# Optimization experiments

Hardware: AMD Instinct MI355X
Metric: run time of the kernel (lower is better)

Reference implementation:

```python
import math
import jax, jax.numpy as jnp
import numpy as np

B, L, S, H, E = 4, 2048, 2048, 8, 64

def setup_inputs() -> dict:
    key = jax.random.key(0)
    kq, kk, kv, km = jax.random.split(key, 4)
    queries = jax.random.normal(kq, (B, L, H, E), dtype=jnp.float32)
    keys = jax.random.normal(kk, (B, S, H, E), dtype=jnp.float32)
    values = jax.random.normal(kv, (B, S, H, E), dtype=jnp.float32)
    # bool mask [B, L, S]; True => masked out (filled with -10000)
    attn_mask = jax.random.randint(km, (B, L, S), 0, 2).astype(bool)
    return {"queries": queries, "keys": keys, "values": values, "attn_mask": attn_mask}

def reference(queries, keys, values, attn_mask):
    # queries: [B,L,H,E], keys/values: [B,S,H,E], attn_mask: [B,L,S] bool
    Edim = queries.shape[-1]
    scale = 1.0 / math.sqrt(Edim)  # self.scale is None -> 1/sqrt(E)
    scores = jnp.einsum('blhe,bshe->bhls', queries, keys) * scale  # [B,H,L,S]
    scores = jnp.where(attn_mask[:, None, :, :], jnp.float32(-10000.0), scores)
    A = jax.nn.softmax(scores, axis=-1)  # dropout is identity at eval time
    V = jnp.einsum('bhls,bshd->blhd', A, values)  # [B,L,H,E]
    return V, A
```

## Files before the change

kernel.cpp:

```cpp
#include <hip/hip_runtime.h>


typedef __attribute__((ext_vector_type(8))) short bf16x8;
typedef __attribute__((ext_vector_type(4))) short bf16x4;
typedef __attribute__((ext_vector_type(4))) float f32x4;

#define NB 4
#define NL 2048
#define NS 2048
#define NH 8
#define NE 64
#define SKC 64
#define SC2 0.18033688011112042f
#define MB2 -5.770780163555854f
#define EXP2(x) __builtin_amdgcn_exp2f(x)

static __device__ __forceinline__ short f2bf(float x) {
  unsigned u = __builtin_bit_cast(unsigned, x);
  u += 0x7fffu + ((u >> 16) & 1u);
  return (short)(u >> 16);
}

static __device__ __forceinline__ bf16x8 pack8(f32x4 a, f32x4 b) {
  bf16x8 t;
  t[0] = f2bf(a[0]); t[1] = f2bf(a[1]); t[2] = f2bf(a[2]); t[3] = f2bf(a[3]);
  t[4] = f2bf(b[0]); t[5] = f2bf(b[1]); t[6] = f2bf(b[2]); t[7] = f2bf(b[3]);
  return t;
}

__global__ __launch_bounds__(256)
void prep_all(const float* __restrict__ K, const float* __restrict__ V,
              const int* __restrict__ M, short* __restrict__ Kb,
              short* __restrict__ Vt, unsigned long long* __restrict__ Mb) {
  __shared__ short t_lds[64 * 65];
  const int bid = blockIdx.x, tid = threadIdx.x;
  if (bid < 4096) {
    long i4 = ((long)bid * 256 + tid) * 4;
    f32x4 v = *(const f32x4*)(K + i4);
    int e4 = (int)(i4 & 63);
    long r = i4 >> 6;
    int h = (int)(r & 7);
    long r2 = r >> 3;
    int t = (int)(r2 & 2047);
    int b = (int)(r2 >> 11);
    bf16x4 o;
    o[0] = f2bf(v[0]); o[1] = f2bf(v[1]); o[2] = f2bf(v[2]); o[3] = f2bf(v[3]);
    *(bf16x4*)(Kb + ((((long)b * NH + h) * NL + t) * NE + e4)) = o;
  } else if (bid < 5120) {
    const int vb = bid - 4096;
    const int b = vb >> 8;
    const int h = (vb >> 5) & 7;
    const int sb = (vb & 31) * 64;
    {
      const int s = tid >> 2, e0 = (tid & 3) * 16;
      const float* vp = V + ((((long)b * NS + sb + s) * NH + h) * NE + e0);
      #pragma unroll
      for (int j = 0; j < 4; ++j) {
        f32x4 u = *(const f32x4*)(vp + j * 4);
        #pragma unroll
        for (int r = 0; r < 4; ++r) t_lds[(e0 + j * 4 + r) * 65 + s] = f2bf(u[r]);
      }
    }
    __syncthreads();
    {
      const int e = tid >> 2, s0 = (tid & 3) * 16;
      short* op = Vt + (((long)b * NH + h) * NE + e) * NS + sb + s0;
      short tmp[16];
      #pragma unroll
      for (int j = 0; j < 16; ++j) tmp[j] = t_lds[e * 65 + s0 + j];
      *(bf16x8*)(op)     = *(bf16x8*)(tmp);
      *(bf16x8*)(op + 8) = *(bf16x8*)(tmp + 8);
    }
  } else {
    const long total = (long)NB * NL * NS;
    long g = (long)(bid - 5120) * 256 + tid;
    const long stride = 2048L * 256;
    for (; g < total; g += stride) {
      unsigned long long bal = __ballot(M[g] != 0);
      if ((tid & 63) == 0) Mb[g >> 6] = bal;
    }
  }
}


template<int RS>
static __device__ __forceinline__ void stage_tile(const short* __restrict__ base,
                                                  short* lds, int tid, int w) {
  #pragma unroll
  for (int c = 0; c < 2; ++c) {
    const int rr = (tid >> 3) + c * 32;
    const int gg = (tid & 7) ^ (rr & 7);
    const short* sp = base + (long)rr * RS + gg * 8;
    __builtin_amdgcn_global_load_lds(
        (const __attribute__((address_space(1))) void*)sp,
        (__attribute__((address_space(3))) void*)(void*)((char*)lds + c * 4096 + w * 1024),
        16, 0, 0);
  }
}

__global__ __launch_bounds__(256, 2)
void attn_main(const float* __restrict__ Qg, const short* __restrict__ Kb,
               const short* __restrict__ Vt, const unsigned long long* __restrict__ Mb,
               float* __restrict__ OutV, float* __restrict__ OutA)
{
  __shared__ short k_lds[2][SKC * 64];
  __shared__ short vt_lds[2][NE * 64];
  __shared__ short p_lds[4][16 * 64];

  const int bid = blockIdx.x;
  const int hh = bid & 7, qt = (bid >> 3) & 15, bb = bid >> 7;
  const int tid = threadIdx.x, w = tid >> 6, lane = tid & 63;
  const int lq = lane & 15, lg = lane >> 4;
  const int qwA = qt * 128 + w * 16, qrowA = qwA + lq;
  const int qwB = qwA + 64,          qrowB = qrowA + 64;

  const short* Kpan = Kb + (long)(bb * NH + hh) * NS * NE;
  const short* Vpan = Vt + (long)(bb * NH + hh) * NE * NS;

  bf16x8 qfA0, qfA1, qfB0, qfB1;
  {
    const float* qp = Qg + (((long)bb * NL + qrowA) * NH + hh) * NE + 8 * lg;
    qfA0 = pack8(*(const f32x4*)(qp),      *(const f32x4*)(qp + 4));
    qfA1 = pack8(*(const f32x4*)(qp + 32), *(const f32x4*)(qp + 36));
    const float* qpB = qp + (long)64 * NH * NE;
    qfB0 = pack8(*(const f32x4*)(qpB),      *(const f32x4*)(qpB + 4));
    qfB1 = pack8(*(const f32x4*)(qpB + 32), *(const f32x4*)(qpB + 36));
  }

  const unsigned long long* mrowA = Mb + ((long)bb * NL + qrowA) * (NS / 64);
  const unsigned long long* mrowB = Mb + ((long)bb * NL + qrowB) * (NS / 64);

  float l0 = 0.f, l1 = 0.f, l2 = 0.f, l3 = 0.f;
  stage_tile<NE>(Kpan, &k_lds[0][0], tid, w);
  __syncthreads();
  unsigned long long mcA = mrowA[0];
  for (int sb = 0; sb < NS; sb += SKC) {
    const int cb = (sb >> 6) & 1;
    if (sb + SKC < NS)
      stage_tile<NE>(Kpan + (long)(sb + SKC) * NE, &k_lds[cb ^ 1][0], tid, w);
    const unsigned long long mnA = (sb + SKC < NS) ? mrowA[(sb >> 6) + 1] : 0ULL;
    #pragma unroll
    for (int st = 0; st < SKC; st += 16) {
      const int krow = st + lq, sw = (krow & 7) << 3;
      const bf16x8 kf0 = *(const bf16x8*)&k_lds[cb][(krow * 64 + 8 * lg) ^ sw];
      const bf16x8 kf1 = *(const bf16x8*)&k_lds[cb][(krow * 64 + 32 + 8 * lg) ^ sw];
      f32x4 c = {0.f, 0.f, 0.f, 0.f};
      c = __builtin_amdgcn_mfma_f32_16x16x32_bf16(kf0, qfA0, c, 0, 0, 0);
      c = __builtin_amdgcn_mfma_f32_16x16x32_bf16(kf1, qfA1, c, 0, 0, 0);
      const unsigned mb4 = (unsigned)(mcA >> (st + 4 * lg)) & 0xFu;
      l0 += (mb4 & 1u) ? 0.f : EXP2(fmaf(c[0], SC2, MB2));
      l1 += (mb4 & 2u) ? 0.f : EXP2(fmaf(c[1], SC2, MB2));
      l2 += (mb4 & 4u) ? 0.f : EXP2(fmaf(c[2], SC2, MB2));
      l3 += (mb4 & 8u) ? 0.f : EXP2(fmaf(c[3], SC2, MB2));
    }
    mcA = mnA;
    __syncthreads();
  }
  float lA = (l0 + l1) + (l2 + l3);
  lA += __shfl_xor(lA, 16, 64);
  lA += __shfl_xor(lA, 32, 64);
  const float rinvA = 1.0f / lA;

  f32x4 accvA[4];
  #pragma unroll
  for (int et = 0; et < 4; ++et) accvA[et] = (f32x4){0.f, 0.f, 0.f, 0.f};
  l0 = l1 = l2 = l3 = 0.f;

  float* arowA = OutA + (((long)(bb * NH + hh)) * NL + qrowA) * NS;

  stage_tile<NE>(Kpan, &k_lds[0][0], tid, w);
  stage_tile<NS>(Vpan, &vt_lds[0][0], tid, w);
  __syncthreads();
  mcA = mrowA[0];
  unsigned long long mcB = mrowB[0];
  for (int sb = 0; sb < NS; sb += SKC) {
    const int cb = (sb >> 6) & 1;
    if (sb + SKC < NS) {
      stage_tile<NE>(Kpan + (long)(sb + SKC) * NE, &k_lds[cb ^ 1][0], tid, w);
      stage_tile<NS>(Vpan + (sb + SKC), &vt_lds[cb ^ 1][0], tid, w);
    }
    const unsigned long long mnA = (sb + SKC < NS) ? mrowA[(sb >> 6) + 1] : 0ULL;
    const unsigned long long mnB = (sb + SKC < NS) ? mrowB[(sb >> 6) + 1] : 0ULL;
    #pragma unroll
    for (int st = 0; st < SKC; st += 16) {
      const int krow = st + lq, sw = (krow & 7) << 3;
      const bf16x8 kf0 = *(const bf16x8*)&k_lds[cb][(krow * 64 + 8 * lg) ^ sw];
      const bf16x8 kf1 = *(const bf16x8*)&k_lds[cb][(krow * 64 + 32 + 8 * lg) ^ sw];
      f32x4 cA = {0.f, 0.f, 0.f, 0.f};
      cA = __builtin_amdgcn_mfma_f32_16x16x32_bf16(kf0, qfA0, cA, 0, 0, 0);
      cA = __builtin_amdgcn_mfma_f32_16x16x32_bf16(kf1, qfA1, cA, 0, 0, 0);
      f32x4 cB = {0.f, 0.f, 0.f, 0.f};
      cB = __builtin_amdgcn_mfma_f32_16x16x32_bf16(kf0, qfB0, cB, 0, 0, 0);
      cB = __builtin_amdgcn_mfma_f32_16x16x32_bf16(kf1, qfB1, cB, 0, 0, 0);
      const unsigned mA4 = (unsigned)(mcA >> (st + 4 * lg)) & 0xFu;
      const float p0 = (mA4 & 1u) ? 0.f : EXP2(fmaf(cA[0], SC2, MB2));
      const float p1 = (mA4 & 2u) ? 0.f : EXP2(fmaf(cA[1], SC2, MB2));
      const float p2 = (mA4 & 4u) ? 0.f : EXP2(fmaf(cA[2], SC2, MB2));
      const float p3 = (mA4 & 8u) ? 0.f : EXP2(fmaf(cA[3], SC2, MB2));
      const float a0 = p0 * rinvA, a1 = p1 * rinvA, a2 = p2 * rinvA, a3 = p3 * rinvA;
      f32x4 av = {a0, a1, a2, a3};
      __builtin_nontemporal_store(av, (f32x4*)(arowA + sb + st + 4 * lg));
      bf16x4 pv;
      pv[0] = f2bf(a0); pv[1] = f2bf(a1); pv[2] = f2bf(a2); pv[3] = f2bf(a3);
      *(bf16x4*)&p_lds[w][(lq * 64 + st + 4 * lg) ^ ((lq & 7) << 3)] = pv;
      const unsigned mB4 = (unsigned)(mcB >> (st + 4 * lg)) & 0xFu;
      l0 += (mB4 & 1u) ? 0.f : EXP2(fmaf(cB[0], SC2, MB2));
      l1 += (mB4 & 2u) ? 0.f : EXP2(fmaf(cB[1], SC2, MB2));
      l2 += (mB4 & 4u) ? 0.f : EXP2(fmaf(cB[2], SC2, MB2));
      l3 += (mB4 & 8u) ? 0.f : EXP2(fmaf(cB[3], SC2, MB2));
    }
    #pragma unroll
    for (int kc2 = 0; kc2 < 2; ++kc2) {
      const bf16x8 pf = *(const bf16x8*)&p_lds[w][(lq * 64 + kc2 * 32 + 8 * lg) ^ ((lq & 7) << 3)];
      #pragma unroll
      for (int et = 0; et < 4; ++et) {
        const int er = et * 16 + lq;
        const bf16x8 vf = *(const bf16x8*)&vt_lds[cb][(er * 64 + kc2 * 32 + 8 * lg) ^ ((er & 7) << 3)];
        accvA[et] = __builtin_amdgcn_mfma_f32_16x16x32_bf16(pf, vf, accvA[et], 0, 0, 0);
      }
    }
    mcA = mnA; mcB = mnB;
    __syncthreads();
  }
  float lB = (l0 + l1) + (l2 + l3);
  lB += __shfl_xor(lB, 16, 64);
  lB += __shfl_xor(lB, 32, 64);
  const float rinvB = 1.0f / lB;

  {
    float* vout = OutV + (((long)bb * NL + qwA + 4 * lg) * NH + hh) * NE + lq;
    #pragma unroll
    for (int r = 0; r < 4; ++r)
      #pragma unroll
      for (int et = 0; et < 4; ++et)
        vout[(long)r * (NH * NE) + et * 16] = accvA[et][r];
  }

  f32x4 accvB[4];
  #pragma unroll
  for (int et = 0; et < 4; ++et) accvB[et] = (f32x4){0.f, 0.f, 0.f, 0.f};

  float* arowB = OutA + (((long)(bb * NH + hh)) * NL + qrowB) * NS;

  stage_tile<NE>(Kpan, &k_lds[0][0], tid, w);
  stage_tile<NS>(Vpan, &vt_lds[0][0], tid, w);
  __syncthreads();
  mcB = mrowB[0];
  for (int sb = 0; sb < NS; sb += SKC) {
    const int cb = (sb >> 6) & 1;
    if (sb + SKC < NS) {
      stage_tile<NE>(Kpan + (long)(sb + SKC) * NE, &k_lds[cb ^ 1][0], tid, w);
      stage_tile<NS>(Vpan + (sb + SKC), &vt_lds[cb ^ 1][0], tid, w);
    }
    const unsigned long long mnB = (sb + SKC < NS) ? mrowB[(sb >> 6) + 1] : 0ULL;
    #pragma unroll
    for (int st = 0; st < SKC; st += 16) {
      const int krow = st + lq, sw = (krow & 7) << 3;
      const bf16x8 kf0 = *(const bf16x8*)&k_lds[cb][(krow * 64 + 8 * lg) ^ sw];
      const bf16x8 kf1 = *(const bf16x8*)&k_lds[cb][(krow * 64 + 32 + 8 * lg) ^ sw];
      f32x4 c = {0.f, 0.f, 0.f, 0.f};
      c = __builtin_amdgcn_mfma_f32_16x16x32_bf16(kf0, qfB0, c, 0, 0, 0);
      c = __builtin_amdgcn_mfma_f32_16x16x32_bf16(kf1, qfB1, c, 0, 0, 0);
      const unsigned mb4 = (unsigned)(mcB >> (st + 4 * lg)) & 0xFu;
      const float p0 = (mb4 & 1u) ? 0.f : EXP2(fmaf(c[0], SC2, MB2));
      const float p1 = (mb4 & 2u) ? 0.f : EXP2(fmaf(c[1], SC2, MB2));
      const float p2 = (mb4 & 4u) ? 0.f : EXP2(fmaf(c[2], SC2, MB2));
      const float p3 = (mb4 & 8u) ? 0.f : EXP2(fmaf(c[3], SC2, MB2));
      const float a0 = p0 * rinvB, a1 = p1 * rinvB, a2 = p2 * rinvB, a3 = p3 * rinvB;
      f32x4 av = {a0, a1, a2, a3};
      __builtin_nontemporal_store(av, (f32x4*)(arowB + sb + st + 4 * lg));
      bf16x4 pv;
      pv[0] = f2bf(a0); pv[1] = f2bf(a1); pv[2] = f2bf(a2); pv[3] = f2bf(a3);
      *(bf16x4*)&p_lds[w][(lq * 64 + st + 4 * lg) ^ ((lq & 7) << 3)] = pv;
    }
    #pragma unroll
    for (int kc2 = 0; kc2 < 2; ++kc2) {
      const bf16x8 pf = *(const bf16x8*)&p_lds[w][(lq * 64 + kc2 * 32 + 8 * lg) ^ ((lq & 7) << 3)];
      #pragma unroll
      for (int et = 0; et < 4; ++et) {
        const int er = et * 16 + lq;
        const bf16x8 vf = *(const bf16x8*)&vt_lds[cb][(er * 64 + kc2 * 32 + 8 * lg) ^ ((er & 7) << 3)];
        accvB[et] = __builtin_amdgcn_mfma_f32_16x16x32_bf16(pf, vf, accvB[et], 0, 0, 0);
      }
    }
    mcB = mnB;
    __syncthreads();
  }

  {
    float* vout = OutV + (((long)bb * NL + qwB + 4 * lg) * NH + hh) * NE + lq;
    #pragma unroll
    for (int r = 0; r < 4; ++r)
      #pragma unroll
      for (int et = 0; et < 4; ++et)
        vout[(long)r * (NH * NE) + et * 16] = accvB[et][r];
  }
}

extern "C" void kernel_launch(void* const* d_in, const int* in_sizes, int n_in,
                              void* d_out, int out_size, void* d_ws, size_t ws_size,
                              hipStream_t stream) {
  const float* Q = (const float*)d_in[0];
  const float* K = (const float*)d_in[1];
  const float* V = (const float*)d_in[2];
  const int*   M = (const int*)d_in[3];
  float* outv = (float*)d_out;
  float* outa = outv + (size_t)NB * NL * NH * NE;

  const size_t NQK = (size_t)NB * NH * NL * NE;
  short* Kbw = (short*)d_ws;
  short* Vtw = Kbw + NQK;
  unsigned long long* Mbp = (unsigned long long*)(Vtw + NQK);

  prep_all<<<dim3(7168), 256, 0, stream>>>(K, V, M, Kbw, Vtw, Mbp);
  attn_main<<<dim3(NB * (NL / 128) * NH), 256, 0, stream>>>(Q, Kbw, Vtw, Mbp, outv, outa);
}
```

Before: 203.1 us.

## Load K and V fragments directly from global memory instead of LDS staging

Removes the double-buffered LDS staging of K and V tiles (global_load_lds plus block barriers) and has each lane read its bf16 MFMA fragments straight from global memory through the cache. This drops the per-iteration __syncthreads and LDS traffic, so warps no longer wait on each other. In exchange every wave re-fetches the same K/V data from L1/L2 with no explicit prefetch, which may expose load latency and raise cache pressure.

```diff
diff --git a/kernel.cpp b/kernel.cpp
--- a/kernel.cpp
+++ b/kernel.cpp
@@ -83,28 +83,11 @@
 }
 
 
-template<int RS>
-static __device__ __forceinline__ void stage_tile(const short* __restrict__ base,
-                                                  short* lds, int tid, int w) {
-  #pragma unroll
-  for (int c = 0; c < 2; ++c) {
-    const int rr = (tid >> 3) + c * 32;
-    const int gg = (tid & 7) ^ (rr & 7);
-    const short* sp = base + (long)rr * RS + gg * 8;
-    __builtin_amdgcn_global_load_lds(
-        (const __attribute__((address_space(1))) void*)sp,
-        (__attribute__((address_space(3))) void*)(void*)((char*)lds + c * 4096 + w * 1024),
-        16, 0, 0);
-  }
-}
-
 __global__ __launch_bounds__(256, 2)
 void attn_main(const float* __restrict__ Qg, const short* __restrict__ Kb,
                const short* __restrict__ Vt, const unsigned long long* __restrict__ Mb,
                float* __restrict__ OutV, float* __restrict__ OutA)
 {
-  __shared__ short k_lds[2][SKC * 64];
-  __shared__ short vt_lds[2][NE * 64];
   __shared__ short p_lds[4][16 * 64];
 
   const int bid = blockIdx.x;
@@ -116,6 +99,9 @@
 
   const short* Kpan = Kb + (long)(bb * NH + hh) * NS * NE;
   const short* Vpan = Vt + (long)(bb * NH + hh) * NE * NS;
+
+  const short* kfrag = Kpan + (long)lq * NE + 8 * lg;
+  const short* vfrag = Vpan + (long)lq * NS + 8 * lg;
 
   bf16x8 qfA0, qfA1, qfB0, qfB1;
   {
@@ -131,19 +117,13 @@
   const unsigned long long* mrowB = Mb + ((long)bb * NL + qrowB) * (NS / 64);
 
   float l0 = 0.f, l1 = 0.f, l2 = 0.f, l3 = 0.f;
-  stage_tile<NE>(Kpan, &k_lds[0][0], tid, w);
-  __syncthreads();
-  unsigned long long mcA = mrowA[0];
   for (int sb = 0; sb < NS; sb += SKC) {
-    const int cb = (sb >> 6) & 1;
-    if (sb + SKC < NS)
-      stage_tile<NE>(Kpan + (long)(sb + SKC) * NE, &k_lds[cb ^ 1][0], tid, w);
-    const unsigned long long mnA = (sb + SKC < NS) ? mrowA[(sb >> 6) + 1] : 0ULL;
+    const unsigned long long mcA = mrowA[sb >> 6];
     #pragma unroll
     for (int st = 0; st < SKC; st += 16) {
-      const int krow = st + lq, sw = (krow & 7) << 3;
-      const bf16x8 kf0 = *(const bf16x8*)&k_lds[cb][(krow * 64 + 8 * lg) ^ sw];
-      const bf16x8 kf1 = *(const bf16x8*)&k_lds[cb][(krow * 64 + 32 + 8 * lg) ^ sw];
+      const short* kp = kfrag + (long)(sb + st) * NE;
+      const bf16x8 kf0 = *(const bf16x8*)(kp);
+      const bf16x8 kf1 = *(const bf16x8*)(kp + 32);
       f32x4 c = {0.f, 0.f, 0.f, 0.f};
       c = __builtin_amdgcn_mfma_f32_16x16x32_bf16(kf0, qfA0, c, 0, 0, 0);
       c = __builtin_amdgcn_mfma_f32_16x16x32_bf16(kf1, qfA1, c, 0, 0, 0);
@@ -153,8 +133,6 @@
       l2 += (mb4 & 4u) ? 0.f : EXP2(fmaf(c[2], SC2, MB2));
       l3 += (mb4 & 8u) ? 0.f : EXP2(fmaf(c[3], SC2, MB2));
     }
-    mcA = mnA;
-    __syncthreads();
   }
   float lA = (l0 + l1) + (l2 + l3);
   lA += __shfl_xor(lA, 16, 64);
@@ -168,24 +146,14 @@
 
   float* arowA = OutA + (((long)(bb * NH + hh)) * NL + qrowA) * NS;
 
-  stage_tile<NE>(Kpan, &k_lds[0][0], tid, w);
-  stage_tile<NS>(Vpan, &vt_lds[0][0], tid, w);
-  __syncthreads();
-  mcA = mrowA[0];
-  unsigned long long mcB = mrowB[0];
   for (int sb = 0; sb < NS; sb += SKC) {
-    const int cb = (sb >> 6) & 1;
-    if (sb + SKC < NS) {
-      stage_tile<NE>(Kpan + (long)(sb + SKC) * NE, &k_lds[cb ^ 1][0], tid, w);
-      stage_tile<NS>(Vpan + (sb + SKC), &vt_lds[cb ^ 1][0], tid, w);
-    }
-    const unsigned long long mnA = (sb + SKC < NS) ? mrowA[(sb >> 6) + 1] : 0ULL;
-    const unsigned long long mnB = (sb + SKC < NS) ? mrowB[(sb >> 6) + 1] : 0ULL;
+    const unsigned long long mcA = mrowA[sb >> 6];
+    const unsigned long long mcB = mrowB[sb >> 6];
     #pragma unroll
     for (int st = 0; st < SKC; st += 16) {
-      const int krow = st + lq, sw = (krow & 7) << 3;
-      const bf16x8 kf0 = *(const bf16x8*)&k_lds[cb][(krow * 64 + 8 * lg) ^ sw];
-      const bf16x8 kf1 = *(const bf16x8*)&k_lds[cb][(krow * 64 + 32 + 8 * lg) ^ sw];
+      const short* kp = kfrag + (long)(sb + st) * NE;
+      const bf16x8 kf0 = *(const bf16x8*)(kp);
+      const bf16x8 kf1 = *(const bf16x8*)(kp + 32);
       f32x4 cA = {0.f, 0.f, 0.f, 0.f};
       cA = __builtin_amdgcn_mfma_f32_16x16x32_bf16(kf0, qfA0, cA, 0, 0, 0);
       cA = __builtin_amdgcn_mfma_f32_16x16x32_bf16(kf1, qfA1, cA, 0, 0, 0);
@@ -214,13 +182,10 @@
       const bf16x8 pf = *(const bf16x8*)&p_lds[w][(lq * 64 + kc2 * 32 + 8 * lg) ^ ((lq & 7) << 3)];
       #pragma unroll
       for (int et = 0; et < 4; ++et) {
-        const int er = et * 16 + lq;
-        const bf16x8 vf = *(const bf16x8*)&vt_lds[cb][(er * 64 + kc2 * 32 + 8 * lg) ^ ((er & 7) << 3)];
+        const bf16x8 vf = *(const bf16x8*)(vfrag + (long)(et * 16) * NS + sb + kc2 * 32);
         accvA[et] = __builtin_amdgcn_mfma_f32_16x16x32_bf16(pf, vf, accvA[et], 0, 0, 0);
       }
     }
-    mcA = mnA; mcB = mnB;
-    __syncthreads();
   }
   float lB = (l0 + l1) + (l2 + l3);
   lB += __shfl_xor(lB, 16, 64);
@@ -242,22 +207,13 @@
 
   float* arowB = OutA + (((long)(bb * NH + hh)) * NL + qrowB) * NS;
 
-  stage_tile<NE>(Kpan, &k_lds[0][0], tid, w);
-  stage_tile<NS>(Vpan, &vt_lds[0][0], tid, w);
-  __syncthreads();
-  mcB = mrowB[0];
   for (int sb = 0; sb < NS; sb += SKC) {
-    const int cb = (sb >> 6) & 1;
-    if (sb + SKC < NS) {
-      stage_tile<NE>(Kpan + (long)(sb + SKC) * NE, &k_lds[cb ^ 1][0], tid, w);
-      stage_tile<NS>(Vpan + (sb + SKC), &vt_lds[cb ^ 1][0], tid, w);
-    }
-    const unsigned long long mnB = (sb + SKC < NS) ? mrowB[(sb >> 6) + 1] : 0ULL;
+    const unsigned long long mcB = mrowB[sb >> 6];
     #pragma unroll
     for (int st = 0; st < SKC; st += 16) {
-      const int krow = st + lq, sw = (krow & 7) << 3;
-      const bf16x8 kf0 = *(const bf16x8*)&k_lds[cb][(krow * 64 + 8 * lg) ^ sw];
-      const bf16x8 kf1 = *(const bf16x8*)&k_lds[cb][(krow * 64 + 32 + 8 * lg) ^ sw];
+      const short* kp = kfrag + (long)(sb + st) * NE;
+      const bf16x8 kf0 = *(const bf16x8*)(kp);
+      const bf16x8 kf1 = *(const bf16x8*)(kp + 32);
       f32x4 c = {0.f, 0.f, 0.f, 0.f};
       c = __builtin_amdgcn_mfma_f32_16x16x32_bf16(kf0, qfB0, c, 0, 0, 0);
       c = __builtin_amdgcn_mfma_f32_16x16x32_bf16(kf1, qfB1, c, 0, 0, 0);
@@ -278,13 +234,10 @@
       const bf16x8 pf = *(const bf16x8*)&p_lds[w][(lq * 64 + kc2 * 32 + 8 * lg) ^ ((lq & 7) << 3)];
       #pragma unroll
       for (int et = 0; et < 4; ++et) {
-        const int er = et * 16 + lq;
-        const bf16x8 vf = *(const bf16x8*)&vt_lds[cb][(er * 64 + kc2 * 32 + 8 * lg) ^ ((er & 7) << 3)];
+        const bf16x8 vf = *(const bf16x8*)(vfrag + (long)(et * 16) * NS + sb + kc2 * 32);
         accvB[et] = __builtin_amdgcn_mfma_f32_16x16x32_bf16(pf, vf, accvB[et], 0, 0, 0);
       }
     }
-    mcB = mnB;
-    __syncthreads();
   }
 
   {
```

Measured after the change: 379.6 us, median of 2. 87.0% more time.

## Triple-buffer K/V LDS tiles with explicit vmcnt waits and raw barriers

Applied to the files above, without the earlier changes.

Turns the double-buffered K and V^T LDS staging into a three-stage ring with prefetch distance two in all three passes. Each iteration issues its loads after the compute and then waits with s_waitcnt vmcnt(N) plus s_barrier, so the newest tile can stay in flight, instead of a full __syncthreads drain. This aims to hide global-load latency behind MFMA and exp work. In exchange, LDS use rises by one K and one V tile per block, and the hand-counted vmcnt values must match the compiler's count of outstanding loads, including the interleaved mask and nontemporal stores, which makes the code fragile.

```diff
diff --git a/kernel.cpp b/kernel.cpp
--- a/kernel.cpp
+++ b/kernel.cpp
@@ -11,6 +11,7 @@
 #define NH 8
 #define NE 64
 #define SKC 64
+#define NT (NS / SKC)
 #define SC2 0.18033688011112042f
 #define MB2 -5.770780163555854f
 #define EXP2(x) __builtin_amdgcn_exp2f(x)
@@ -103,8 +104,8 @@
                const short* __restrict__ Vt, const unsigned long long* __restrict__ Mb,
                float* __restrict__ OutV, float* __restrict__ OutA)
 {
-  __shared__ short k_lds[2][SKC * 64];
-  __shared__ short vt_lds[2][NE * 64];
+  __shared__ short k_lds[3][SKC * 64];
+  __shared__ short vt_lds[3][NE * 64];
   __shared__ short p_lds[4][16 * 64];
 
   const int bid = blockIdx.x;
@@ -131,30 +132,39 @@
   const unsigned long long* mrowB = Mb + ((long)bb * NL + qrowB) * (NS / 64);
 
   float l0 = 0.f, l1 = 0.f, l2 = 0.f, l3 = 0.f;
-  stage_tile<NE>(Kpan, &k_lds[0][0], tid, w);
-  __syncthreads();
-  unsigned long long mcA = mrowA[0];
-  for (int sb = 0; sb < NS; sb += SKC) {
-    const int cb = (sb >> 6) & 1;
-    if (sb + SKC < NS)
-      stage_tile<NE>(Kpan + (long)(sb + SKC) * NE, &k_lds[cb ^ 1][0], tid, w);
-    const unsigned long long mnA = (sb + SKC < NS) ? mrowA[(sb >> 6) + 1] : 0ULL;
-    #pragma unroll
-    for (int st = 0; st < SKC; st += 16) {
-      const int krow = st + lq, sw = (krow & 7) << 3;
-      const bf16x8 kf0 = *(const bf16x8*)&k_lds[cb][(krow * 64 + 8 * lg) ^ sw];
-      const bf16x8 kf1 = *(const bf16x8*)&k_lds[cb][(krow * 64 + 32 + 8 * lg) ^ sw];
-      f32x4 c = {0.f, 0.f, 0.f, 0.f};
-      c = __builtin_amdgcn_mfma_f32_16x16x32_bf16(kf0, qfA0, c, 0, 0, 0);
-      c = __builtin_amdgcn_mfma_f32_16x16x32_bf16(kf1, qfA1, c, 0, 0, 0);
-      const unsigned mb4 = (unsigned)(mcA >> (st + 4 * lg)) & 0xFu;
-      l0 += (mb4 & 1u) ? 0.f : EXP2(fmaf(c[0], SC2, MB2));
-      l1 += (mb4 & 2u) ? 0.f : EXP2(fmaf(c[1], SC2, MB2));
-      l2 += (mb4 & 4u) ? 0.f : EXP2(fmaf(c[2], SC2, MB2));
-      l3 += (mb4 & 8u) ? 0.f : EXP2(fmaf(c[3], SC2, MB2));
-    }
-    mcA = mnA;
-    __syncthreads();
+  {
+    short *k0 = &k_lds[0][0], *k1 = &k_lds[1][0], *k2 = &k_lds[2][0];
+    stage_tile<NE>(Kpan, k0, tid, w);
+    stage_tile<NE>(Kpan + (long)SKC * NE, k1, tid, w);
+    asm volatile("s_waitcnt vmcnt(2)" ::: "memory");
+    __builtin_amdgcn_s_barrier();
+    unsigned long long mcA = mrowA[0];
+    for (int t = 0; t < NT; ++t) {
+      const unsigned long long mnA = mrowA[t + 1 < NT ? t + 1 : NT - 1];
+      #pragma unroll
+      for (int st = 0; st < SKC; st += 16) {
+        const int krow = st + lq, sw = (krow & 7) << 3;
+        const bf16x8 kf0 = *(const bf16x8*)&k0[(krow * 64 + 8 * lg) ^ sw];
+        const bf16x8 kf1 = *(const bf16x8*)&k0[(krow * 64 + 32 + 8 * lg) ^ sw];
+        f32x4 c = {0.f, 0.f, 0.f, 0.f};
+        c = __builtin_amdgcn_mfma_f32_16x16x32_bf16(kf0, qfA0, c, 0, 0, 0);
+        c = __builtin_amdgcn_mfma_f32_16x16x32_bf16(kf1, qfA1, c, 0, 0, 0);
+        const unsigned mb4 = (unsigned)(mcA >> (st + 4 * lg)) & 0xFu;
+        l0 += (mb4 & 1u) ? 0.f : EXP2(fmaf(c[0], SC2, MB2));
+        l1 += (mb4 & 2u) ? 0.f : EXP2(fmaf(c[1], SC2, MB2));
+        l2 += (mb4 & 4u) ? 0.f : EXP2(fmaf(c[2], SC2, MB2));
+        l3 += (mb4 & 8u) ? 0.f : EXP2(fmaf(c[3], SC2, MB2));
+      }
+      mcA = mnA;
+      if (t + 2 < NT) {
+        stage_tile<NE>(Kpan + (long)(t + 2) * SKC * NE, k2, tid, w);
+        asm volatile("s_waitcnt vmcnt(2)" ::: "memory");
+      } else {
+        asm volatile("s_waitcnt vmcnt(0)" ::: "memory");
+      }
+      __builtin_amdgcn_s_barrier();
+      short* tmp = k0; k0 = k1; k1 = k2; k2 = tmp;
+    }
   }
   float lA = (l0 + l1) + (l2 + l3);
   lA += __shfl_xor(lA, 16, 64);
@@ -167,60 +177,70 @@
   l0 = l1 = l2 = l3 = 0.f;
 
   float* arowA = OutA + (((long)(bb * NH + hh)) * NL + qrowA) * NS;
-
-  stage_tile<NE>(Kpan, &k_lds[0][0], tid, w);
-  stage_tile<NS>(Vpan, &vt_lds[0][0], tid, w);
-  __syncthreads();
-  mcA = mrowA[0];
-  unsigned long long mcB = mrowB[0];
-  for (int sb = 0; sb < NS; sb += SKC) {
-    const int cb = (sb >> 6) & 1;
-    if (sb + SKC < NS) {
-      stage_tile<NE>(Kpan + (long)(sb + SKC) * NE, &k_lds[cb ^ 1][0], tid, w);
-      stage_tile<NS>(Vpan + (sb + SKC), &vt_lds[cb ^ 1][0], tid, w);
-    }
-    const unsigned long long mnA = (sb + SKC < NS) ? mrowA[(sb >> 6) + 1] : 0ULL;
-    const unsigned long long mnB = (sb + SKC < NS) ? mrowB[(sb >> 6) + 1] : 0ULL;
-    #pragma unroll
-    for (int st = 0; st < SKC; st += 16) {
-      const int krow = st + lq, sw = (krow & 7) << 3;
-      const bf16x8 kf0 = *(const bf16x8*)&k_lds[cb][(krow * 64 + 8 * lg) ^ sw];
-      const bf16x8 kf1 = *(const bf16x8*)&k_lds[cb][(krow * 64 + 32 + 8 * lg) ^ sw];
-      f32x4 cA = {0.f, 0.f, 0.f, 0.f};
-      cA = __builtin_amdgcn_mfma_f32_16x16x32_bf16(kf0, qfA0, cA, 0, 0, 0);
-      cA = __builtin_amdgcn_mfma_f32_16x16x32_bf16(kf1, qfA1, cA, 0, 0, 0);
-      f32x4 cB = {0.f, 0.f, 0.f, 0.f};
-      cB = __builtin_amdgcn_mfma_f32_16x16x32_bf16(kf0, qfB0, cB, 0, 0, 0);
-      cB = __builtin_amdgcn_mfma_f32_16x16x32_bf16(kf1, qfB1, cB, 0, 0, 0);
-      const unsigned mA4 = (unsigned)(mcA >> (st + 4 * lg)) & 0xFu;
-      const float p0 = (mA4 & 1u) ? 0.f : EXP2(fmaf(cA[0], SC2, MB2));
-      const float p1 = (mA4 & 2u) ? 0.f : EXP2(fmaf(cA[1], SC2, MB2));
-      const float p2 = (mA4 & 4u) ? 0.f : EXP2(fmaf(cA[2], SC2, MB2));
-      const float p3 = (mA4 & 8u) ? 0.f : EXP2(fmaf(cA[3], SC2, MB2));
-      const float a0 = p0 * rinvA, a1 = p1 * rinvA, a2 = p2 * rinvA, a3 = p3 * rinvA;
-      f32x4 av = {a0, a1, a2, a3};
-      __builtin_nontemporal_store(av, (f32x4*)(arowA + sb + st + 4 * lg));
-      bf16x4 pv;
-      pv[0] = f2bf(a0); pv[1] = f2bf(a1); pv[2] = f2bf(a2); pv[3] = f2bf(a3);
-      *(bf16x4*)&p_lds[w][(lq * 64 + st + 4 * lg) ^ ((lq & 7) << 3)] = pv;
-      const unsigned mB4 = (unsigned)(mcB >> (st + 4 * lg)) & 0xFu;
-      l0 += (mB4 & 1u) ? 0.f : EXP2(fmaf(cB[0], SC2, MB2));
-      l1 += (mB4 & 2u) ? 0.f : EXP2(fmaf(cB[1], SC2, MB2));
-      l2 += (mB4 & 4u) ? 0.f : EXP2(fmaf(cB[2], SC2, MB2));
-      l3 += (mB4 & 8u) ? 0.f : EXP2(fmaf(cB[3], SC2, MB2));
-    }
-    #pragma unroll
-    for (int kc2 = 0; kc2 < 2; ++kc2) {
-      const bf16x8 pf = *(const bf16x8*)&p_lds[w][(lq * 64 + kc2 * 32 + 8 * lg) ^ ((lq & 7) << 3)];
-      #pragma unroll
-      for (int et = 0; et < 4; ++et) {
-        const int er = et * 16 + lq;
-        const bf16x8 vf = *(const bf16x8*)&vt_lds[cb][(er * 64 + kc2 * 32 + 8 * lg) ^ ((er & 7) << 3)];
-        accvA[et] = __builtin_amdgcn_mfma_f32_16x16x32_bf16(pf, vf, accvA[et], 0, 0, 0);
-      }
-    }
-    mcA = mnA; mcB = mnB;
-    __syncthreads();
+  {
+    short *k0 = &k_lds[0][0], *k1 = &k_lds[1][0], *k2 = &k_lds[2][0];
+    short *v0 = &vt_lds[0][0], *v1 = &vt_lds[1][0], *v2 = &vt_lds[2][0];
+    stage_tile<NE>(Kpan, k0, tid, w);
+    stage_tile<NS>(Vpan, v0, tid, w);
+    stage_tile<NE>(Kpan + (long)SKC * NE, k1, tid, w);
+    stage_tile<NS>(Vpan + SKC, v1, tid, w);
+    asm volatile("s_waitcnt vmcnt(4)" ::: "memory");
+    __builtin_amdgcn_s_barrier();
+    unsigned long long mcA = mrowA[0], mcB = mrowB[0];
+    for (int t = 0; t < NT; ++t) {
+      const int tn = t + 1 < NT ? t + 1 : NT - 1;
+      const unsigned long long mnA = mrowA[tn], mnB = mrowB[tn];
+      const int sb = t * SKC;
+      #pragma unroll
+      for (int st = 0; st < SKC; st += 16) {
+        const int krow = st + lq, sw = (krow & 7) << 3;
+        const bf16x8 kf0 = *(const bf16x8*)&k0[(krow * 64 + 8 * lg) ^ sw];
+        const bf16x8 kf1 = *(const bf16x8*)&k0[(krow * 64 + 32 + 8 * lg) ^ sw];
+        f32x4 cA = {0.f, 0.f, 0.f, 0.f};
+        cA = __builtin_amdgcn_mfma_f32_16x16x32_bf16(kf0, qfA0, cA, 0, 0, 0);
+        cA = __builtin_amdgcn_mfma_f32_16x16x32_bf16(kf1, qfA1, cA, 0, 0, 0);
+        f32x4 cB = {0.f, 0.f, 0.f, 0.f};
+        cB = __builtin_amdgcn_mfma_f32_16x16x32_bf16(kf0, qfB0, cB, 0, 0, 0);
+        cB = __builtin_amdgcn_mfma_f32_16x16x32_bf16(kf1, qfB1, cB, 0, 0, 0);
+        const unsigned mA4 = (unsigned)(mcA >> (st + 4 * lg)) & 0xFu;
+        const float p0 = (mA4 & 1u) ? 0.f : EXP2(fmaf(cA[0], SC2, MB2));
+        const float p1 = (mA4 & 2u) ? 0.f : EXP2(fmaf(cA[1], SC2, MB2));
+        const float p2 = (mA4 & 4u) ? 0.f : EXP2(fmaf(cA[2], SC2, MB2));
+        const float p3 = (mA4 & 8u) ? 0.f : EXP2(fmaf(cA[3], SC2, MB2));
+        const float a0 = p0 * rinvA, a1 = p1 * rinvA, a2 = p2 * rinvA, a3 = p3 * rinvA;
+        f32x4 av = {a0, a1, a2, a3};
+        __builtin_nontemporal_store(av, (f32x4*)(arowA + sb + st + 4 * lg));
+        bf16x4 pv;
+        pv[0] = f2bf(a0); pv[1] = f2bf(a1); pv[2] = f2bf(a2); pv[3] = f2bf(a3);
+        *(bf16x4*)&p_lds[w][(lq * 64 + st + 4 * lg) ^ ((lq & 7) << 3)] = pv;
+        const unsigned mB4 = (unsigned)(mcB >> (st + 4 * lg)) & 0xFu;
+        l0 += (mB4 & 1u) ? 0.f : EXP2(fmaf(cB[0], SC2, MB2));
+        l1 += (mB4 & 2u) ? 0.f : EXP2(fmaf(cB[1], SC2, MB2));
+        l2 += (mB4 & 4u) ? 0.f : EXP2(fmaf(cB[2], SC2, MB2));
+        l3 += (mB4 & 8u) ? 0.f : EXP2(fmaf(cB[3], SC2, MB2));
+      }
+      #pragma unroll
+      for (int kc2 = 0; kc2 < 2; ++kc2) {
+        const bf16x8 pf = *(const bf16x8*)&p_lds[w][(lq * 64 + kc2 * 32 + 8 * lg) ^ ((lq & 7) << 3)];
+        #pragma unroll
+        for (int et = 0; et < 4; ++et) {
+          const int er = et * 16 + lq;
+          const bf16x8 vf = *(const bf16x8*)&v0[(er * 64 + kc2 * 32 + 8 * lg) ^ ((er & 7) << 3)];
+          accvA[et] = __builtin_amdgcn_mfma_f32_16x16x32_bf16(pf, vf, accvA[et], 0, 0, 0);
+        }
+      }
+      mcA = mnA; mcB = mnB;
+      if (t + 2 < NT) {
+        stage_tile<NE>(Kpan + (long)(t + 2) * SKC * NE, k2, tid, w);
+        stage_tile<NS>(Vpan + (t + 2) * SKC, v2, tid, w);
+        asm volatile("s_waitcnt vmcnt(4)" ::: "memory");
+      } else {
+        asm volatile("s_waitcnt vmcnt(0)" ::: "memory");
+      }
+      __builtin_amdgcn_s_barrier();
+      short* tk = k0; k0 = k1; k1 = k2; k2 = tk;
+      short* tv = v0; v0 = v1; v1 = v2; v2 = tv;
+    }
   }
   float lB = (l0 + l1) + (l2 + l3);
   lB += __shfl_xor(lB, 16, 64);
@@ -241,50 +261,61 @@
   for (int et = 0; et < 4; ++et) accvB[et] = (f32x4){0.f, 0.f, 0.f, 0.f};
 
   float* arowB = OutA + (((long)(bb * NH + hh)) * NL + qrowB) * NS;
-
-  stage_tile<NE>(Kpan, &k_lds[0][0], tid, w);
-  stage_tile<NS>(Vpan, &vt_lds[0][0], tid, w);
-  __syncthreads();
-  mcB = mrowB[0];
-  for (int sb = 0; sb < NS; sb += SKC) {
-    const int cb = (sb >> 6) & 1;
-    if (sb + SKC < NS) {
-      stage_tile<NE>(Kpan + (long)(sb + SKC) * NE, &k_lds[cb ^ 1][0], tid, w);
-      stage_tile<NS>(Vpan + (sb + SKC), &vt_lds[cb ^ 1][0], tid, w);
-    }
-    const unsigned long long mnB = (sb + SKC < NS) ? mrowB[(sb >> 6) + 1] : 0ULL;
-    #pragma unroll
-    for (int st = 0; st < SKC; st += 16) {
-      const int krow = st + lq, sw = (krow & 7) << 3;
-      const bf16x8 kf0 = *(const bf16x8*)&k_lds[cb][(krow * 64 + 8 * lg) ^ sw];
-      const bf16x8 kf1 = *(const bf16x8*)&k_lds[cb][(krow * 64 + 32 + 8 * lg) ^ sw];
-      f32x4 c = {0.f, 0.f, 0.f, 0.f};
-      c = __builtin_amdgcn_mfma_f32_16x16x32_bf16(kf0, qfB0, c, 0, 0, 0);
-      c = __builtin_amdgcn_mfma_f32_16x16x32_bf16(kf1, qfB1, c, 0, 0, 0);
-      const unsigned mb4 = (unsigned)(mcB >> (st + 4 * lg)) & 0xFu;
-      const float p0 = (mb4 & 1u) ? 0.f : EXP2(fmaf(c[0], SC2, MB2));
-      const float p1 = (mb4 & 2u) ? 0.f : EXP2(fmaf(c[1], SC2, MB2));
-      const float p2 = (mb4 & 4u) ? 0.f : EXP2(fmaf(c[2], SC2, MB2));
-      const float p3 = (mb4 & 8u) ? 0.f : EXP2(fmaf(c[3], SC2, MB2));
-      const float a0 = p0 * rinvB, a1 = p1 * rinvB, a2 = p2 * rinvB, a3 = p3 * rinvB;
-      f32x4 av = {a0, a1, a2, a3};
-      __builtin_nontemporal_store(av, (f32x4*)(arowB + sb + st + 4 * lg));
-      bf16x4 pv;
-      pv[0] = f2bf(a0); pv[1] = f2bf(a1); pv[2] = f2bf(a2); pv[3] = f2bf(a3);
-      *(bf16x4*)&p_lds[w][(lq * 64 + st + 4 * lg) ^ ((lq & 7) << 3)] = pv;
-    }
-    #pragma unroll
-    for (int kc2 = 0; kc2 < 2; ++kc2) {
-      const bf16x8 pf = *(const bf16x8*)&p_lds[w][(lq * 64 + kc2 * 32 + 8 * lg) ^ ((lq & 7) << 3)];
-      #pragma unroll
-      for (int et = 0; et < 4; ++et) {
-        const int er = et * 16 + lq;
-        const bf16x8 vf = *(const bf16x8*)&vt_lds[cb][(er * 64 + kc2 * 32 + 8 * lg) ^ ((er & 7) << 3)];
-        accvB[et] = __builtin_amdgcn_mfma_f32_16x16x32_bf16(pf, vf, accvB[et], 0, 0, 0);
-      }
-    }
-    mcB = mnB;
-    __syncthreads();
+  {
+    short *k0 = &k_lds[0][0], *k1 = &k_lds[1][0], *k2 = &k_lds[2][0];
+    short *v0 = &vt_lds[0][0], *v1 = &vt_lds[1][0], *v2 = &vt_lds[2][0];
+    stage_tile<NE>(Kpan, k0, tid, w);
+    stage_tile<NS>(Vpan, v0, tid, w);
+    stage_tile<NE>(Kpan + (long)SKC * NE, k1, tid, w);
+    stage_tile<NS>(Vpan + SKC, v1, tid, w);
+    asm volatile("s_waitcnt vmcnt(4)" ::: "memory");
+    __builtin_amdgcn_s_barrier();
+    unsigned long long mcB = mrowB[0];
+    for (int t = 0; t < NT; ++t) {
+      const unsigned long long mnB = mrowB[t + 1 < NT ? t + 1 : NT - 1];
+      const int sb = t * SKC;
+      #pragma unroll
+      for (int st = 0; st < SKC; st += 16) {
+        const int krow = st + lq, sw = (krow & 7) << 3;
+        const bf16x8 kf0 = *(const bf16x8*)&k0[(krow * 64 + 8 * lg) ^ sw];
+        const bf16x8 kf1 = *(const bf16x8*)&k0[(krow * 64 + 32 + 8 * lg) ^ sw];
+        f32x4 c = {0.f, 0.f, 0.f, 0.f};
+        c = __builtin_amdgcn_mfma_f32_16x16x32_bf16(kf0, qfB0, c, 0, 0, 0);
+        c = __builtin_amdgcn_mfma_f32_16x16x32_bf16(kf1, qfB1, c, 0, 0, 0);
+        const unsigned mb4 = (unsigned)(mcB >> (st + 4 * lg)) & 0xFu;
+        const float p0 = (mb4 & 1u) ? 0.f : EXP2(fmaf(c[0], SC2, MB2));
+        const float p1 = (mb4 & 2u) ? 0.f : EXP2(fmaf(c[1], SC2, MB2));
+        const float p2 = (mb4 & 4u) ? 0.f : EXP2(fmaf(c[2], SC2, MB2));
+        const float p3 = (mb4 & 8u) ? 0.f : EXP2(fmaf(c[3], SC2, MB2));
+        const float a0 = p0 * rinvB, a1 = p1 * rinvB, a2 = p2 * rinvB, a3 = p3 * rinvB;
+        f32x4 av = {a0, a1, a2, a3};
+        __builtin_nontemporal_store(av, (f32x4*)(arowB + sb + st + 4 * lg));
+        bf16x4 pv;
+        pv[0] = f2bf(a0); pv[1] = f2bf(a1); pv[2] = f2bf(a2); pv[3] = f2bf(a3);
+        *(bf16x4*)&p_lds[w][(lq * 64 + st + 4 * lg) ^ ((lq & 7) << 3)] = pv;
+      }
+      #pragma unroll
+      for (int kc2 = 0; kc2 < 2; ++kc2) {
+        const bf16x8 pf = *(const bf16x8*)&p_lds[w][(lq * 64 + kc2 * 32 + 8 * lg) ^ ((lq & 7) << 3)];
+        #pragma unroll
+        for (int et = 0; et < 4; ++et) {
+          const int er = et * 16 + lq;
+          const bf16x8 vf = *(const bf16x8*)&v0[(er * 64 + kc2 * 32 + 8 * lg) ^ ((er & 7) << 3)];
+          accvB[et] = __builtin_amdgcn_mfma_f32_16x16x32_bf16(pf, vf, accvB[et], 0, 0, 0);
+        }
+      }
+      mcB = mnB;
+      if (t + 2 < NT) {
+        stage_tile<NE>(Kpan + (long)(t + 2) * SKC * NE, k2, tid, w);
+        stage_tile<NS>(Vpan + (t + 2) * SKC, v2, tid, w);
+        asm volatile("s_waitcnt vmcnt(4)" ::: "memory");
+      } else {
+        asm volatile("s_waitcnt vmcnt(0)" ::: "memory");
+      }
+      __builtin_amdgcn_s_barrier();
+      short* tk = k0; k0 = k1; k1 = k2; k2 = tk;
+      short* tv = v0; v0 = v1; v1 = v2; v2 = tv;
+    }
   }
 
   {
```

Result: faster. 195.1 us (-3.9%).
